# Kernel tuning notes

Measured on AMD Instinct MI355X. Metric: run time of the kernel, lower is better.

## Reference

```python
import jax, jax.numpy as jnp
import numpy as np

IN_NC = 32
OUT_NC = 32
HIDDEN = 192  # in_nc * expand_ratio(6)
KS = 3
EPS = 1e-5


def setup_inputs() -> dict:
    key = jax.random.key(0)
    k1, k2 = jax.random.split(key)
    b, h, w = 8, 128, 128
    fh = fw = 8
    hyper = IN_NC * HIDDEN + HIDDEN * KS * KS + HIDDEN * OUT_NC  # 14016
    return {
        "x": jax.random.normal(k1, (b, IN_NC, h, w), jnp.float32),
        "s": jax.random.normal(k2, (b, hyper, fh, fw), jnp.float32),
        "g1": jnp.ones((HIDDEN,), jnp.float32),
        "b1": jnp.zeros((HIDDEN,), jnp.float32),
        "g2": jnp.ones((HIDDEN,), jnp.float32),
        "b2": jnp.zeros((HIDDEN,), jnp.float32),
        "g3": jnp.ones((OUT_NC,), jnp.float32),
        "b3": jnp.zeros((OUT_NC,), jnp.float32),
    }


def _bn(x, gamma, beta):
    # x: [P, H, W, C]; training-mode BatchNorm2d over (P, H, W) per channel
    mean = jnp.mean(x, axis=(0, 1, 2))
    var = jnp.var(x, axis=(0, 1, 2))  # biased, matches torch normalization
    return (x - mean) * jax.lax.rsqrt(var + EPS) * gamma + beta


def _relu6(x):
    return jnp.clip(x, 0.0, 6.0)


def _forward(x, s, g1, b1, g2, b2, g3, b3):
    b, c, h, w = x.shape
    fh, fw = s.shape[-2], s.shape[-1]
    ph, pw = h // fh, w // fw
    kh, kw = ph + 2, pw + 2  # padding (1,1)

    # reflect-pad then unfold into per-patch tiles [P, kh, kw, c]
    xp = jnp.pad(x, ((0, 0), (0, 0), (1, 1), (1, 1)), mode="reflect")
    xp = xp.transpose(0, 2, 3, 1)  # [b, h+2, w+2, c]
    ih = jnp.arange(fh)[:, None] * ph + jnp.arange(kh)[None, :]  # [fh, kh]
    iw = jnp.arange(fw)[:, None] * pw + jnp.arange(kw)[None, :]  # [fw, kw]
    t = xp[:, ih]            # [b, fh, kh, w+2, c]
    t = t[:, :, :, iw]       # [b, fh, kh, fw, kw, c]
    patches = t.transpose(0, 1, 3, 2, 4, 5).reshape(b * fh * fw, kh, kw, c)

    # per-patch hypernet weights
    wt = s.transpose(0, 2, 3, 1).reshape(b * fh * fw, -1)  # [P, hyper]
    r1 = IN_NC * HIDDEN
    r2 = r1 + HIDDEN * KS * KS
    w1 = wt[:, :r1].reshape(-1, HIDDEN, IN_NC)          # pointwise expand
    w2 = wt[:, r1:r2].reshape(-1, HIDDEN, KS, KS)        # depthwise 3x3
    w3 = wt[:, r2:].reshape(-1, OUT_NC, HIDDEN)          # pointwise project

    # 1x1 expand + BN + ReLU6
    x1 = jnp.einsum("pijc,poc->pijo", patches, w1)       # [P, kh, kw, hidden]
    x1 = _relu6(_bn(x1, g1, b1))

    # depthwise 3x3 (valid, stride 1) + BN + ReLU6
    ii = jnp.arange(ph)[:, None] + jnp.arange(KS)[None, :]
    jj = jnp.arange(pw)[:, None] + jnp.arange(KS)[None, :]
    win = x1[:, ii]          # [P, ph, 3, kw, hidden]
    win = win[:, :, :, jj]   # [P, ph, 3, pw, 3, hidden]
    x2 = jnp.einsum("piujvc,pcuv->pijc", win, w2)        # [P, ph, pw, hidden]
    x2 = _relu6(_bn(x2, g2, b2))

    # 1x1 project + BN
    x3 = jnp.einsum("pijc,poc->pijo", x2, w3)            # [P, ph, pw, out]
    x3 = _bn(x3, g3, b3)

    out = x3.reshape(b, fh, fw, ph, pw, OUT_NC)
    out = out.transpose(0, 5, 1, 3, 2, 4).reshape(b, OUT_NC, h, w)
    return x + out  # use_res_connect: stride==1 and in_nc==out_nc


def reference(x, s, g1, b1, g2, b2, g3, b3):
    return _forward(x, s, g1, b1, g2, b2, g3, b3)
```

## Files before the change

### kernel.cpp

```cpp
#include <hip/hip_runtime.h>

#define EPS 1e-5f

namespace {
constexpr int HYPER = 14016;
constexpr int HID   = 192;
constexpr int A1    = 324;
constexpr int A2    = 256;
constexpr int P_TOT = 512;
constexpr int W1SZ  = 6144;
constexpr int WT2SZ = 7872;
constexpr int R3OFF = 1728;

constexpr size_t WB1_B = 0;
constexpr size_t WT2_B = 6291456;
constexpr size_t X2_B  = WT2_B + 16121856;
constexpr size_t X3_B  = X2_B + 50331648;
constexpr size_t SUM_B = X3_B + 8388608;
constexpr int REP = 832;
}

typedef __attribute__((ext_vector_type(8))) short bf16x8;
typedef __attribute__((ext_vector_type(4))) float f32x4;
typedef __attribute__((ext_vector_type(4))) unsigned int u32x4;

__device__ __forceinline__ float relu6f(float v) { return fminf(fmaxf(v, 0.f), 6.f); }

__device__ __forceinline__ float bf2f(unsigned int h) {
  return __uint_as_float(h << 16);
}
__device__ __forceinline__ unsigned short f2bf(float f) {
  unsigned int u = __float_as_uint(f);
  return (unsigned short)((u + 0x7FFFu + ((u >> 16) & 1u)) >> 16);
}

__device__ __forceinline__ float rsum4(const float* __restrict__ base, int idx) {
  return ((base[idx] + base[REP + idx]) + (base[2 * REP + idx] + base[3 * REP + idx]));
}

__device__ __host__ __forceinline__ int afrag_slot(int o, int c) {
  return (o >> 4) * 512 + (c >> 3) * 128 + (o & 15) * 8 + (c & 7);
}

__global__ __launch_bounds__(256) void k0_transpose(const float* __restrict__ s,
                                                    unsigned short* __restrict__ wb1,
                                                    float* __restrict__ wt2) {
  __shared__ float tile[64][65];
  const int blk = blockIdx.x;
  const int b  = blk / 219;
  const int kt = blk - b * 219;
  const int k0 = kt * 64;
  const int t  = threadIdx.x;
  {
    const int f  = t & 63;
    const int kr = t >> 6;
    const float* sp = s + ((size_t)b * HYPER + k0 + kr) * 64 + f;
#pragma unroll
    for (int kk = 0; kk < 16; kk++)
      tile[kr + kk * 4][f] = sp[(size_t)kk * 4 * 64];
  }
  __syncthreads();
  {
    const int kk = t & 63;
    const int fr = t >> 6;
    if (kt < 96) {
      const int k = k0 + kk;
      const int o = k >> 5, c = k & 31;
      const int slot = afrag_slot(o, c);
      unsigned short* wp = wb1 + ((size_t)b * 64 + fr) * W1SZ + slot;
#pragma unroll
      for (int ff = 0; ff < 16; ff++)
        wp[(size_t)ff * 4 * W1SZ] = f2bf(tile[kk][fr + ff * 4]);
    } else {
      float* wp = wt2 + ((size_t)b * 64 + fr) * WT2SZ + (k0 - W1SZ) + kk;
#pragma unroll
      for (int ff = 0; ff < 16; ff++)
        wp[(size_t)ff * 4 * WT2SZ] = tile[kk][fr + ff * 4];
    }
  }
}

__global__ __launch_bounds__(512) void k1_stats(const float* __restrict__ x,
                                                const unsigned short* __restrict__ wb1,
                                                float* __restrict__ sums) {
  __shared__ __align__(16) unsigned short pL[21 * 512];
  __shared__ float stat[384];
  const int p  = blockIdx.x;
  const int b  = p >> 6;
  const int fi = (p >> 3) & 7;
  const int fj = p & 7;
  const int t  = threadIdx.x;

  if (t < 384) stat[t] = 0.f;

  const int row0 = fi * 16 - 1, col0 = fj * 16 - 1;
  const float* xb = x + (size_t)b * 32 * 128 * 128;
  for (int idx = t; idx < 32 * A1; idx += 512) {
    int c  = idx / A1;
    int ij = idx - c * A1;
    int ii = ij / 18;
    int jj = ij - ii * 18;
    int r  = row0 + ii; r  = (r  < 0) ? 1 : (r  > 127) ? 126 : r;
    int cl = col0 + jj; cl = (cl < 0) ? 1 : (cl > 127) ? 126 : cl;
    int slot = ((ij >> 4) * 4 + (c >> 3)) * 128 + (ij & 15) * 8 + (c & 7);
    pL[slot] = f2bf(xb[((size_t)c * 128 + r) * 128 + cl]);
  }
  __syncthreads();

  const int lane = t & 63;
  const int wv   = t >> 6;
  const int m16  = lane & 15;
  const int quad = lane >> 4;
  const int jh   = wv & 1;
  const int wo   = wv >> 1;
  const int jt0  = jh ? 11 : 0;
  const int jt1  = jh ? 21 : 11;
  const unsigned short* wbp = wb1 + (size_t)p * W1SZ;

  for (int oi = 0; oi < 3; oi++) {
    const int ot = wo + oi * 4;
    bf16x8 a = *(const bf16x8*)(wbp + ot * 512 + lane * 8);
    float sacc[4] = {0.f, 0.f, 0.f, 0.f};
    float qacc[4] = {0.f, 0.f, 0.f, 0.f};
    for (int jt = jt0; jt < jt1; jt++) {
      bf16x8 bb = *(const bf16x8*)&pL[jt * 512 + lane * 8];
      f32x4 d = __builtin_amdgcn_mfma_f32_16x16x32_bf16(a, bb, (f32x4){0.f, 0.f, 0.f, 0.f}, 0, 0, 0);
      const int ij = jt * 16 + m16;
      if (ij < A1) {
#pragma unroll
        for (int r = 0; r < 4; r++) {
          float v = d[r];
          sacc[r] += v;
          qacc[r] = fmaf(v, v, qacc[r]);
        }
      }
    }
#pragma unroll
    for (int r = 0; r < 4; r++) {
      float sv = sacc[r], qv = qacc[r];
#pragma unroll
      for (int msk = 1; msk < 16; msk <<= 1) {
        sv += __shfl_xor(sv, msk, 64);
        qv += __shfl_xor(qv, msk, 64);
      }
      if (m16 == 0) {
        int o = ot * 16 + quad * 4 + r;
        atomicAdd(&stat[o], sv);
        atomicAdd(&stat[192 + o], qv);
      }
    }
  }
  __syncthreads();
  if (t < 384) atomicAdd(&sums[(p & 3) * REP + t], stat[t]);
}

__global__ __launch_bounds__(512, 4) void k2_fused(const float* __restrict__ x,
                                                   const unsigned short* __restrict__ wb1,
                                                   const float* __restrict__ wt2,
                                                   const float* __restrict__ sums,
                                                   const float* __restrict__ g1,
                                                   const float* __restrict__ b1,
                                                   unsigned short* __restrict__ x2,
                                                   float* __restrict__ sums_out) {
  __shared__ __align__(16) unsigned short pL[21 * 512];
  __shared__ __align__(16) unsigned short xc[16 * 328];
  __shared__ __align__(16) unsigned short x2s[256 * 18];
  __shared__ float w2L[HID * 9];
  __shared__ float sc[HID], sh[HID];
  __shared__ float st2[384];
  const int p  = blockIdx.x;
  const int b  = p >> 6;
  const int fi = (p >> 3) & 7;
  const int fj = p & 7;
  const int t  = threadIdx.x;

  const float inv1 = 1.f / 165888.f;
  if (t < HID) {
    float m   = rsum4(sums, t) * inv1;
    float var = rsum4(sums, 192 + t) * inv1 - m * m;
    float scl = g1[t] * rsqrtf(var + EPS);
    sc[t] = scl;
    sh[t] = b1[t] - m * scl;
  }
  if (t < 384) st2[t] = 0.f;
  {
    const float* wtp = wt2 + (size_t)p * WT2SZ;
    for (int i = t; i < HID * 9; i += 512) w2L[i] = wtp[i];
  }

  const int row0 = fi * 16 - 1, col0 = fj * 16 - 1;
  const float* xb = x + (size_t)b * 32 * 128 * 128;
  for (int idx = t; idx < 32 * A1; idx += 512) {
    int c  = idx / A1;
    int ij = idx - c * A1;
    int ii = ij / 18;
    int jj = ij - ii * 18;
    int r  = row0 + ii; r  = (r  < 0) ? 1 : (r  > 127) ? 126 : r;
    int cl = col0 + jj; cl = (cl < 0) ? 1 : (cl > 127) ? 126 : cl;
    int slot = ((ij >> 4) * 4 + (c >> 3)) * 128 + (ij & 15) * 8 + (c & 7);
    pL[slot] = f2bf(xb[((size_t)c * 128 + r) * 128 + cl]);
  }
  __syncthreads();

  const int lane = t & 63;
  const int wv   = t >> 6;
  const int m16  = lane & 15;
  const int quad = lane >> 4;
  const int ihq = t >> 7;
  const int cdw = (t >> 3) & 15;
  const int jp  = t & 7;
  const unsigned short* wbp = wb1 + (size_t)p * W1SZ;
  unsigned short* x2base = x2 + (size_t)p * 49152;

  auto conv1 = [&](int rt) {
    bf16x8 a = *(const bf16x8*)(wbp + rt * 512 + lane * 8);
    float scv[4], shv[4];
#pragma unroll
    for (int r = 0; r < 4; r++) {
      scv[r] = sc[rt * 16 + quad * 4 + r];
      shv[r] = sh[rt * 16 + quad * 4 + r];
    }
    for (int jt = wv; jt < 21; jt += 8) {
      bf16x8 bb = *(const bf16x8*)&pL[jt * 512 + lane * 8];
      f32x4 d = __builtin_amdgcn_mfma_f32_16x16x32_bf16(a, bb, (f32x4){0.f, 0.f, 0.f, 0.f}, 0, 0, 0);
      const int ij = jt * 16 + m16;
      if (ij < A1) {
#pragma unroll
        for (int r = 0; r < 4; r++) {
          float v = relu6f(fmaf(d[r], scv[r], shv[r]));
          unsigned int u;
          asm("v_cvt_pk_bf16_f32 %0, %1, %2" : "=v"(u) : "v"(v), "v"(v));
          xc[(quad * 4 + r) * 328 + ij] = (unsigned short)u;
        }
      }
    }
  };

  conv1(0);
  __syncthreads();

  for (int rt = 0; rt < 12; rt++) {
    {
      const int ch = rt * 16 + cdw;
      float wr[9];
#pragma unroll
      for (int u = 0; u < 9; u++) wr[u] = w2L[ch * 9 + u];
      float a0[4], a1[4];
#pragma unroll
      for (int i = 0; i < 4; i++) { a0[i] = 0.f; a1[i] = 0.f; }
      const unsigned short* xcc = &xc[cdw * 328];
#pragma unroll
      for (int rr = 0; rr < 6; rr++) {
        const int rg = ihq * 4 + rr;
        unsigned int d0 = *(const unsigned int*)&xcc[rg * 18 + jp * 2];
        unsigned int d1 = *(const unsigned int*)&xcc[rg * 18 + jp * 2 + 2];
        float v0 = bf2f(d0 & 0xFFFFu), v1 = bf2f(d0 >> 16);
        float v2 = bf2f(d1 & 0xFFFFu), v3 = bf2f(d1 >> 16);
#pragma unroll
        for (int u = 0; u < 3; u++) {
          int il = rr - u;
          if (il >= 0 && il < 4) {
            a0[il] = fmaf(v0, wr[u * 3 + 0], fmaf(v1, wr[u * 3 + 1], fmaf(v2, wr[u * 3 + 2], a0[il])));
            a1[il] = fmaf(v1, wr[u * 3 + 0], fmaf(v2, wr[u * 3 + 1], fmaf(v3, wr[u * 3 + 2], a1[il])));
          }
        }
      }
      float ls = 0.f, lq = 0.f;
#pragma unroll
      for (int il = 0; il < 4; il++) {
        const int ig = ihq * 4 + il;
        const int j0 = jp * 2;
        unsigned int ua;
        asm("v_cvt_pk_bf16_f32 %0, %1, %2" : "=v"(ua) : "v"(a0[il]), "v"(a1[il]));
        float s0 = __uint_as_float(ua << 16);
        float s1 = __uint_as_float(ua & 0xFFFF0000u);
        ls += s0 + s1;
        lq = fmaf(s0, s0, fmaf(s1, s1, lq));
        x2s[(ig * 16 + j0) * 18 + cdw]     = (unsigned short)ua;
        x2s[(ig * 16 + j0 + 1) * 18 + cdw] = (unsigned short)(ua >> 16);
      }
      ls += __shfl_xor(ls, 1, 64); lq += __shfl_xor(lq, 1, 64);
      ls += __shfl_xor(ls, 2, 64); lq += __shfl_xor(lq, 2, 64);
      ls += __shfl_xor(ls, 4, 64); lq += __shfl_xor(lq, 4, 64);
      if (jp == 0) {
        atomicAdd(&st2[ch], ls);
        atomicAdd(&st2[192 + ch], lq);
      }
    }
    __syncthreads();
    {
      unsigned short* dst = x2base + (size_t)rt * 4096;
#pragma unroll
      for (int k = 0; k < 2; k++) {
        int g  = (k * 512 + t) * 4;
        int ij = g >> 4, c0 = g & 15;
        unsigned int v0 = *(const unsigned int*)&x2s[ij * 18 + c0];
        unsigned int v1 = *(const unsigned int*)&x2s[ij * 18 + c0 + 2];
        uint2 v; v.x = v0; v.y = v1;
        *(uint2*)&dst[g] = v;
      }
    }
    if (rt < 11) conv1(rt + 1);
    __syncthreads();
  }
  for (int i = t; i < 384; i += 512) atomicAdd(&sums_out[(p & 3) * REP + 384 + i], st2[i]);
}

__global__ __launch_bounds__(256) void k3_pw2(const unsigned short* __restrict__ x2,
                                              const float* __restrict__ wt2,
                                              const float* __restrict__ sums,
                                              const float* __restrict__ g2,
                                              const float* __restrict__ b2,
                                              unsigned short* __restrict__ x3,
                                              float* __restrict__ sums_out) {
  __shared__ __align__(16) unsigned short wA[12 * 512];
  __shared__ float sc[HID], sh[HID];
  __shared__ float st3[64];
  const int blk  = blockIdx.x;
  const int p    = blk >> 1;
  const int half = blk & 1;
  const int t    = threadIdx.x;
  const float inv = 1.f / 131072.f;
  for (int c = t; c < HID; c += 256) {
    float m   = rsum4(sums, 384 + c) * inv;
    float var = rsum4(sums, 576 + c) * inv - m * m;
    float scl = g2[c] * rsqrtf(var + EPS);
    sc[c] = scl;
    sh[c] = b2[c] - m * scl;
  }
  if (t < 64) st3[t] = 0.f;
  const float* w3p = wt2 + (size_t)p * WT2SZ + R3OFF;
  for (int idx = t; idx < 32 * 48; idx += 256) {
    int o  = idx / 48;
    int c4 = idx - o * 48;
    float4 v = *(const float4*)&w3p[o * HID + c4 * 4];
    int slot = ((o >> 4) * 6 + (c4 >> 3)) * 512 + ((((c4 >> 1) & 3) * 16) + (o & 15)) * 8 + (c4 & 1) * 4;
    ushort4 u;
    u.x = f2bf(v.x); u.y = f2bf(v.y); u.z = f2bf(v.z); u.w = f2bf(v.w);
    *(ushort4*)&wA[slot] = u;
  }
  __syncthreads();
  const int lane = t & 63;
  const int wv   = t >> 6;
  const int m16  = lane & 15;
  const int kg   = lane >> 4;
  bf16x8 aF[2][6];
#pragma unroll
  for (int ot = 0; ot < 2; ot++)
#pragma unroll
    for (int ks = 0; ks < 6; ks++)
      aF[ot][ks] = *(const bf16x8*)&wA[(ot * 6 + ks) * 512 + lane * 8];
  const unsigned short* x2p = x2 + (size_t)p * 12 * 4096;
  f32x4 acc[2][2];
#pragma unroll
  for (int it = 0; it < 2; it++)
#pragma unroll
    for (int ot = 0; ot < 2; ot++)
#pragma unroll
      for (int r = 0; r < 4; r++) acc[it][ot][r] = 0.f;
#pragma unroll
  for (int it = 0; it < 2; it++) {
    const int ijt = half * 8 + wv + it * 4;
    const int ij  = ijt * 16 + m16;
    const unsigned short* brow = x2p + (size_t)(kg >> 1) * 4096 + (size_t)ij * 16 + (kg & 1) * 8;
#pragma unroll
    for (int ks = 0; ks < 6; ks++) {
      u32x4 uv = *(const u32x4*)&brow[ks * 8192];
      const float* scp = &sc[ks * 32 + kg * 8];
      const float* shp = &sh[ks * 32 + kg * 8];
      u32x4 pk;
#pragma unroll
      for (int q = 0; q < 4; q++) {
        float ylo = relu6f(fmaf(__uint_as_float(uv[q] << 16),          scp[2 * q],     shp[2 * q]));
        float yhi = relu6f(fmaf(__uint_as_float(uv[q] & 0xFFFF0000u),  scp[2 * q + 1], shp[2 * q + 1]));
        unsigned int r;
        asm("v_cvt_pk_bf16_f32 %0, %1, %2" : "=v"(r) : "v"(ylo), "v"(yhi));
        pk[q] = r;
      }
      bf16x8 bb = __builtin_bit_cast(bf16x8, pk);
      acc[it][0] = __builtin_amdgcn_mfma_f32_16x16x32_bf16(aF[0][ks], bb, acc[it][0], 0, 0, 0);
      acc[it][1] = __builtin_amdgcn_mfma_f32_16x16x32_bf16(aF[1][ks], bb, acc[it][1], 0, 0, 0);
    }
  }
  unsigned short* x3p = x3 + (size_t)p * 32 * A2;
  float sacc[2][4] = {{0.f}}, qacc[2][4] = {{0.f}};
#pragma unroll
  for (int it = 0; it < 2; it++) {
    const int ijt = half * 8 + wv + it * 4;
#pragma unroll
    for (int ot = 0; ot < 2; ot++) {
#pragma unroll
      for (int rp = 0; rp < 2; rp++) {
        unsigned int ua;
        asm("v_cvt_pk_bf16_f32 %0, %1, %2" : "=v"(ua)
            : "v"(acc[it][ot][2 * rp]), "v"(acc[it][ot][2 * rp + 1]));
        float v0 = __uint_as_float(ua << 16);
        float v1 = __uint_as_float(ua & 0xFFFF0000u);
        x3p[(size_t)(ot * 16 + kg * 4 + 2 * rp) * A2 + ijt * 16 + m16]     = (unsigned short)ua;
        x3p[(size_t)(ot * 16 + kg * 4 + 2 * rp + 1) * A2 + ijt * 16 + m16] = (unsigned short)(ua >> 16);
        sacc[ot][2 * rp]     += v0;
        sacc[ot][2 * rp + 1] += v1;
        qacc[ot][2 * rp]      = fmaf(v0, v0, qacc[ot][2 * rp]);
        qacc[ot][2 * rp + 1]  = fmaf(v1, v1, qacc[ot][2 * rp + 1]);
      }
    }
  }
#pragma unroll
  for (int ot = 0; ot < 2; ot++)
#pragma unroll
    for (int r = 0; r < 4; r++) {
      float sv = sacc[ot][r], qv = qacc[ot][r];
#pragma unroll
      for (int msk = 1; msk < 16; msk <<= 1) {
        sv += __shfl_xor(sv, msk, 64);
        qv += __shfl_xor(qv, msk, 64);
      }
      if (m16 == 0) {
        int o = ot * 16 + kg * 4 + r;
        atomicAdd(&st3[o], sv);
        atomicAdd(&st3[32 + o], qv);
      }
    }
  __syncthreads();
  if (t < 64) atomicAdd(&sums_out[(blk & 3) * REP + 768 + t], st3[t]);
}

__global__ __launch_bounds__(256) void k4_out(const float* __restrict__ x,
                                              const unsigned short* __restrict__ x3,
                                              const float* __restrict__ sums,
                                              const float* __restrict__ g3,
                                              const float* __restrict__ b3,
                                              float* __restrict__ out) {
  const int idx4 = blockIdx.x * 256 + threadIdx.x;
  const int w4 = idx4 & 31;
  int tmp = idx4 >> 5;
  const int h = tmp & 127; tmp >>= 7;
  const int o = tmp & 31;
  const int b = tmp >> 5;
  const int fi = h >> 4, i = h & 15;
  const int fj = w4 >> 2;
  const int j0 = (w4 & 3) * 4;
  const int p   = b * 64 + fi * 8 + fj;
  const int ij0 = i * 16 + j0;
  const float inv = 1.f / 131072.f;
  float m   = rsum4(sums, 768 + o) * inv;
  float var = rsum4(sums, 800 + o) * inv - m * m;
  float sv  = g3[o] * rsqrtf(var + EPS);
  float shv = b3[o] - m * sv;
  float4 xv = *(const float4*)&x[(size_t)idx4 * 4];
  ushort4 u = *(const ushort4*)&x3[((size_t)p * 32 + o) * A2 + ij0];
  float4 r;
  r.x = fmaf(bf2f(u.x), sv, shv) + xv.x;
  r.y = fmaf(bf2f(u.y), sv, shv) + xv.y;
  r.z = fmaf(bf2f(u.z), sv, shv) + xv.z;
  r.w = fmaf(bf2f(u.w), sv, shv) + xv.w;
  *(float4*)&out[(size_t)idx4 * 4] = r;
}

extern "C" void kernel_launch(void* const* d_in, const int* in_sizes, int n_in,
                              void* d_out, int out_size, void* d_ws, size_t ws_size,
                              hipStream_t stream) {
  const float* x  = (const float*)d_in[0];
  const float* s  = (const float*)d_in[1];
  const float* g1 = (const float*)d_in[2];
  const float* b1 = (const float*)d_in[3];
  const float* g2 = (const float*)d_in[4];
  const float* b2 = (const float*)d_in[5];
  const float* g3 = (const float*)d_in[6];
  const float* b3 = (const float*)d_in[7];
  char* base = (char*)d_ws;
  unsigned short* wb1  = (unsigned short*)(base + WB1_B);
  float*          wt2  = (float*)(base + WT2_B);
  unsigned short* x2   = (unsigned short*)(base + X2_B);
  unsigned short* x3   = (unsigned short*)(base + X3_B);
  float*          sums = (float*)(base + SUM_B);
  float* out = (float*)d_out;

  hipMemsetAsync(sums, 0, 4 * REP * sizeof(float), stream);
  k0_transpose<<<8 * 219, 256, 0, stream>>>(s, wb1, wt2);
  k1_stats<<<P_TOT, 512, 0, stream>>>(x, wb1, sums);
  k2_fused<<<P_TOT, 512, 0, stream>>>(x, wb1, wt2, sums, g1, b1, x2, sums);
  k3_pw2<<<1024, 256, 0, stream>>>(x2, wt2, sums, g2, b2, x3, sums);
  k4_out<<<4096, 256, 0, stream>>>(x, x3, sums, g3, b3, out);
}
```

Baseline: 184.5 us.

## Compute BN1 statistics via per-patch Gram matrix instead of full expand GEMM

The first-stage BatchNorm statistics are now derived algebraically. Each patch computes a 32x32 Gram matrix of its input tile and the per-channel input sums, then forms each hidden channel's sum as w·S and its sum of squares as wᵀGw. This replaces the full 192-output expand GEMM over the patch pixels with a much smaller 32x32 GEMM plus a small per-output quadratic form. The atomic reduction replicas also grow from 4 to 16 to cut contention, so every consumer now sums 16 partials and the memset clears a larger buffer.

Result: faster. 179.7 us (-2.6%).

```diff
diff --git a/kernel.cpp b/kernel.cpp
--- a/kernel.cpp
+++ b/kernel.cpp
@@ -17,7 +17,8 @@
 constexpr size_t X2_B  = WT2_B + 16121856;
 constexpr size_t X3_B  = X2_B + 50331648;
 constexpr size_t SUM_B = X3_B + 8388608;
-constexpr int REP = 832;
+constexpr int REP  = 832;
+constexpr int NREP = 16;
 }
 
 typedef __attribute__((ext_vector_type(8))) short bf16x8;
@@ -34,12 +35,20 @@
   return (unsigned short)((u + 0x7FFFu + ((u >> 16) & 1u)) >> 16);
 }
 
-__device__ __forceinline__ float rsum4(const float* __restrict__ base, int idx) {
-  return ((base[idx] + base[REP + idx]) + (base[2 * REP + idx] + base[3 * REP + idx]));
+__device__ __forceinline__ float rsum16(const float* __restrict__ base, int idx) {
+  float s = 0.f;
+#pragma unroll
+  for (int r = 0; r < NREP; r++) s += base[r * REP + idx];
+  return s;
 }
 
 __device__ __host__ __forceinline__ int afrag_slot(int o, int c) {
   return (o >> 4) * 512 + (c >> 3) * 128 + (o & 15) * 8 + (c & 7);
+}
+
+__device__ __forceinline__ int gfrag_slot(int c, int ij) {
+  const int ks = ij >> 5, il = ij & 31;
+  return ks * 1024 + (c >> 4) * 512 + (il >> 3) * 128 + (c & 15) * 8 + (il & 7);
 }
 
 __global__ __launch_bounds__(256) void k0_transpose(const float* __restrict__ s,
@@ -83,16 +92,20 @@
 __global__ __launch_bounds__(512) void k1_stats(const float* __restrict__ x,
                                                 const unsigned short* __restrict__ wb1,
                                                 float* __restrict__ sums) {
-  __shared__ __align__(16) unsigned short pL[21 * 512];
-  __shared__ float stat[384];
+  __shared__ __align__(16) unsigned short pG[11 * 1024];
+  __shared__ float G[32 * 32];
+  __shared__ float S[32];
   const int p  = blockIdx.x;
   const int b  = p >> 6;
   const int fi = (p >> 3) & 7;
   const int fj = p & 7;
   const int t  = threadIdx.x;
 
-  if (t < 384) stat[t] = 0.f;
-
+  for (int idx = t; idx < 32 * 28; idx += 512) {
+    int c  = idx / 28;
+    int ij = 324 + (idx - c * 28);
+    pG[gfrag_slot(c, ij)] = 0;
+  }
   const int row0 = fi * 16 - 1, col0 = fj * 16 - 1;
   const float* xb = x + (size_t)b * 32 * 128 * 128;
   for (int idx = t; idx < 32 * A1; idx += 512) {
@@ -102,8 +115,7 @@
     int jj = ij - ii * 18;
     int r  = row0 + ii; r  = (r  < 0) ? 1 : (r  > 127) ? 126 : r;
     int cl = col0 + jj; cl = (cl < 0) ? 1 : (cl > 127) ? 126 : cl;
-    int slot = ((ij >> 4) * 4 + (c >> 3)) * 128 + (ij & 15) * 8 + (c & 7);
-    pL[slot] = f2bf(xb[((size_t)c * 128 + r) * 128 + cl]);
+    pG[gfrag_slot(c, ij)] = f2bf(xb[((size_t)c * 128 + r) * 128 + cl]);
   }
   __syncthreads();
 
@@ -111,47 +123,61 @@
   const int wv   = t >> 6;
   const int m16  = lane & 15;
   const int quad = lane >> 4;
-  const int jh   = wv & 1;
-  const int wo   = wv >> 1;
-  const int jt0  = jh ? 11 : 0;
-  const int jt1  = jh ? 21 : 11;
-  const unsigned short* wbp = wb1 + (size_t)p * W1SZ;
-
-  for (int oi = 0; oi < 3; oi++) {
-    const int ot = wo + oi * 4;
-    bf16x8 a = *(const bf16x8*)(wbp + ot * 512 + lane * 8);
-    float sacc[4] = {0.f, 0.f, 0.f, 0.f};
-    float qacc[4] = {0.f, 0.f, 0.f, 0.f};
-    for (int jt = jt0; jt < jt1; jt++) {
-      bf16x8 bb = *(const bf16x8*)&pL[jt * 512 + lane * 8];
-      f32x4 d = __builtin_amdgcn_mfma_f32_16x16x32_bf16(a, bb, (f32x4){0.f, 0.f, 0.f, 0.f}, 0, 0, 0);
-      const int ij = jt * 16 + m16;
-      if (ij < A1) {
-#pragma unroll
-        for (int r = 0; r < 4; r++) {
-          float v = d[r];
-          sacc[r] += v;
-          qacc[r] = fmaf(v, v, qacc[r]);
-        }
-      }
-    }
-#pragma unroll
-    for (int r = 0; r < 4; r++) {
-      float sv = sacc[r], qv = qacc[r];
-#pragma unroll
-      for (int msk = 1; msk < 16; msk <<= 1) {
-        sv += __shfl_xor(sv, msk, 64);
-        qv += __shfl_xor(qv, msk, 64);
-      }
-      if (m16 == 0) {
-        int o = ot * 16 + quad * 4 + r;
-        atomicAdd(&stat[o], sv);
-        atomicAdd(&stat[192 + o], qv);
-      }
-    }
-  }
-  __syncthreads();
-  if (t < 384) atomicAdd(&sums[(p & 3) * REP + t], stat[t]);
+
+  if (wv < 4) {
+    const int mi = wv >> 1, ni = wv & 1;
+    f32x4 acc = {0.f, 0.f, 0.f, 0.f};
+    for (int ks = 0; ks < 11; ks++) {
+      bf16x8 a  = *(const bf16x8*)&pG[ks * 1024 + mi * 512 + lane * 8];
+      bf16x8 bv = *(const bf16x8*)&pG[ks * 1024 + ni * 512 + lane * 8];
+      acc = __builtin_amdgcn_mfma_f32_16x16x32_bf16(a, bv, acc, 0, 0, 0);
+    }
+#pragma unroll
+    for (int r = 0; r < 4; r++)
+      G[(mi * 16 + quad * 4 + r) * 32 + ni * 16 + m16] = acc[r];
+  } else {
+    const int idx = t - 256;
+    const int c   = idx >> 3;
+    const int k8  = idx & 7;
+    float sv = 0.f;
+    for (int ij = k8; ij < A1; ij += 8)
+      sv += bf2f(pG[gfrag_slot(c, ij)]);
+    sv += __shfl_xor(sv, 1, 64);
+    sv += __shfl_xor(sv, 2, 64);
+    sv += __shfl_xor(sv, 4, 64);
+    if (k8 == 0) S[c] = sv;
+  }
+  __syncthreads();
+
+  if (t < HID) {
+    const int o = t;
+    const unsigned short* wp = wb1 + (size_t)p * W1SZ + (o >> 4) * 512 + (o & 15) * 8;
+    float w[32];
+#pragma unroll
+    for (int c8 = 0; c8 < 4; c8++) {
+      bf16x8 v = *(const bf16x8*)(wp + c8 * 128);
+#pragma unroll
+      for (int j = 0; j < 8; j++)
+        w[c8 * 8 + j] = bf2f((unsigned short)v[j]);
+    }
+    float s1 = 0.f, q1 = 0.f;
+#pragma unroll
+    for (int c = 0; c < 32; c++) {
+      float inner = 0.f;
+#pragma unroll
+      for (int d4 = 0; d4 < 8; d4++) {
+        f32x4 g = *(const f32x4*)&G[c * 32 + d4 * 4];
+        inner = fmaf(g[0], w[d4 * 4 + 0], inner);
+        inner = fmaf(g[1], w[d4 * 4 + 1], inner);
+        inner = fmaf(g[2], w[d4 * 4 + 2], inner);
+        inner = fmaf(g[3], w[d4 * 4 + 3], inner);
+      }
+      q1 = fmaf(w[c], inner, q1);
+      s1 = fmaf(w[c], S[c], s1);
+    }
+    atomicAdd(&sums[(p & (NREP - 1)) * REP + o], s1);
+    atomicAdd(&sums[(p & (NREP - 1)) * REP + 192 + o], q1);
+  }
 }
 
 __global__ __launch_bounds__(512, 4) void k2_fused(const float* __restrict__ x,
@@ -176,8 +202,8 @@
 
   const float inv1 = 1.f / 165888.f;
   if (t < HID) {
-    float m   = rsum4(sums, t) * inv1;
-    float var = rsum4(sums, 192 + t) * inv1 - m * m;
+    float m   = rsum16(sums, t) * inv1;
+    float var = rsum16(sums, 192 + t) * inv1 - m * m;
     float scl = g1[t] * rsqrtf(var + EPS);
     sc[t] = scl;
     sh[t] = b1[t] - m * scl;
@@ -303,7 +329,8 @@
     if (rt < 11) conv1(rt + 1);
     __syncthreads();
   }
-  for (int i = t; i < 384; i += 512) atomicAdd(&sums_out[(p & 3) * REP + 384 + i], st2[i]);
+  for (int i = t; i < 384; i += 512)
+    atomicAdd(&sums_out[(p & (NREP - 1)) * REP + 384 + i], st2[i]);
 }
 
 __global__ __launch_bounds__(256) void k3_pw2(const unsigned short* __restrict__ x2,
@@ -322,8 +349,8 @@
   const int t    = threadIdx.x;
   const float inv = 1.f / 131072.f;
   for (int c = t; c < HID; c += 256) {
-    float m   = rsum4(sums, 384 + c) * inv;
-    float var = rsum4(sums, 576 + c) * inv - m * m;
+    float m   = rsum16(sums, 384 + c) * inv;
+    float var = rsum16(sums, 576 + c) * inv - m * m;
     float scl = g2[c] * rsqrtf(var + EPS);
     sc[c] = scl;
     sh[c] = b2[c] - m * scl;
@@ -422,7 +449,7 @@
       }
     }
   __syncthreads();
-  if (t < 64) atomicAdd(&sums_out[(blk & 3) * REP + 768 + t], st3[t]);
+  if (t < 64) atomicAdd(&sums_out[(blk & (NREP - 1)) * REP + 768 + t], st3[t]);
 }
 
 __global__ __launch_bounds__(256) void k4_out(const float* __restrict__ x,
@@ -443,8 +470,8 @@
   const int p   = b * 64 + fi * 8 + fj;
   const int ij0 = i * 16 + j0;
   const float inv = 1.f / 131072.f;
-  float m   = rsum4(sums, 768 + o) * inv;
-  float var = rsum4(sums, 800 + o) * inv - m * m;
+  float m   = rsum16(sums, 768 + o) * inv;
+  float var = rsum16(sums, 800 + o) * inv - m * m;
   float sv  = g3[o] * rsqrtf(var + EPS);
   float shv = b3[o] - m * sv;
   float4 xv = *(const float4*)&x[(size_t)idx4 * 4];
@@ -476,7 +503,7 @@
   float*          sums = (float*)(base + SUM_B);
   float* out = (float*)d_out;
 
-  hipMemsetAsync(sums, 0, 4 * REP * sizeof(float), stream);
+  hipMemsetAsync(sums, 0, NREP * REP * sizeof(float), stream);
   k0_transpose<<<8 * 219, 256, 0, stream>>>(s, wb1, wt2);
   k1_stats<<<P_TOT, 512, 0, stream>>>(x, wb1, sums);
   k2_fused<<<P_TOT, 512, 0, stream>>>(x, wb1, wt2, sums, g1, b1, x2, sums);
```
